# Kernel tuning notes

Hardware: AMD Instinct MI355X
Metric: run time of the kernel (lower is better)

## Reference

```python
import jax, jax.numpy as jnp
import numpy as np

DIM = 2048
N_HEADS = 16
HEAD_DIM = DIM // N_HEADS
B, S = 2, 2048


def apply_rotary(x, cos, sin):
    # x: [..., dim]; cos/sin broadcast to [..., dim//2]
    # even/odd interleaved rotation, matching the torch ::2 / 1::2 indexing
    xe = x[..., 0::2]
    xo = x[..., 1::2]
    oe = xe * cos - xo * sin
    oo = xo * cos + xe * sin
    return jnp.stack([oe, oo], axis=-1).reshape(x.shape)


def setup_inputs() -> dict:
    key = jax.random.key(0)
    ks = jax.random.split(key, 12)
    scale = 1.0 / np.sqrt(DIM)
    x = jax.random.normal(ks[0], (B, S, DIM), dtype=jnp.float32)
    cos = jax.random.normal(ks[1], (S, DIM // 2), dtype=jnp.float32)
    sin = jax.random.normal(ks[2], (S, DIM // 2), dtype=jnp.float32)
    mask = jnp.zeros((1, 1, S, S), dtype=jnp.float32)
    Wq = jax.random.normal(ks[3], (DIM, DIM), dtype=jnp.float32) * scale
    bq = jnp.zeros((DIM,), dtype=jnp.float32)
    Wk = jax.random.normal(ks[4], (DIM, DIM), dtype=jnp.float32) * scale
    bk = jnp.zeros((DIM,), dtype=jnp.float32)
    Wv = jax.random.normal(ks[5], (DIM, DIM), dtype=jnp.float32) * scale
    bv = jnp.zeros((DIM,), dtype=jnp.float32)
    Wo = jax.random.normal(ks[6], (DIM, DIM), dtype=jnp.float32) * scale
    bo = jnp.zeros((DIM,), dtype=jnp.float32)
    return {"x": x, "cos": cos, "sin": sin, "mask": mask,
            "Wq": Wq, "bq": bq, "Wk": Wk, "bk": bk,
            "Wv": Wv, "bv": bv, "Wo": Wo, "bo": bo}


def reference(x, cos, sin, mask, Wq, bq, Wk, bk, Wv, bv, Wo, bo):
    # Linear projections (torch nn.Linear: y = x @ W.T + b)
    q = jnp.einsum('bsd,ed->bse', x, Wq) + bq
    k = jnp.einsum('bsd,ed->bse', x, Wk) + bk
    v = jnp.einsum('bsd,ed->bse', x, Wv) + bv
    # RoPE on full dim, then split into heads (faithful to source ordering)
    q = apply_rotary(q, cos, sin).reshape(B, S, N_HEADS, HEAD_DIM)
    k = apply_rotary(k, cos, sin).reshape(B, S, N_HEADS, HEAD_DIM)
    v = v.reshape(B, S, N_HEADS, HEAD_DIM)
    scale = 1.0 / jnp.sqrt(jnp.float32(HEAD_DIM))
    attn = jnp.einsum('bqhd,bkhd->bhqk', q, k) * scale  # [B,H,S,S]
    attn = attn + mask
    attn = jax.nn.softmax(attn, axis=-1)
    out = jnp.einsum('bhqk,bkhd->bqhd', attn, v).reshape(B, S, DIM)
    return jnp.einsum('bsd,ed->bse', out, Wo) + bo
```

## Files before the change

### kernel.cpp

```cpp
#include <hip/hip_runtime.h>

#define DIM   2048
#define SLEN  2048
#define BATCH 2
#define NHEAD 16
#define HDIM  128
#define MROWS (BATCH*SLEN)

typedef __attribute__((ext_vector_type(8))) __bf16 bf16x8;
typedef __attribute__((ext_vector_type(4))) float  f32x4;
typedef __attribute__((ext_vector_type(8))) unsigned short u16x8;
typedef __attribute__((ext_vector_type(4))) unsigned short u16x4;

__device__ __forceinline__ unsigned short f2bf(float f) {
  union { float f; unsigned u; } v; v.f = f;
  unsigned r = v.u + 0x7FFFu + ((v.u >> 16) & 1u);
  return (unsigned short)(r >> 16);
}
__device__ __forceinline__ float bf2f(unsigned short h) {
  union { unsigned u; float f; } v; v.u = ((unsigned)h) << 16;
  return v.f;
}
__device__ __forceinline__ void gload16(const void* g, void* l) {
  __builtin_amdgcn_global_load_lds(
      (const __attribute__((address_space(1))) void*)g,
      (__attribute__((address_space(3))) void*)l, 16, 0, 0);
}

__global__ __launch_bounds__(256) void conv_f32_bf16(
    const float* __restrict__ in, unsigned short* __restrict__ out, int n4) {
  int t = blockIdx.x * 256 + threadIdx.x;
  if (t >= n4) return;
  f32x4 v = *(const f32x4*)(in + (size_t)t * 4);
  u16x4 o;
  o[0] = f2bf(v[0]); o[1] = f2bf(v[1]); o[2] = f2bf(v[2]); o[3] = f2bf(v[3]);
  *(u16x4*)(out + (size_t)t * 4) = o;
}

template<int OUT_MODE>
__global__ __launch_bounds__(256) void gemm_bt(
    const unsigned short* __restrict__ A,
    const unsigned short* __restrict__ Bw,
    const float* __restrict__ bias,
    void* __restrict__ Cout, int M, int N, int K)
{
  __shared__ __align__(16) unsigned short As[128][32];
  __shared__ __align__(16) unsigned short Bs[128][32];
  const int tid  = threadIdx.x;
  const int lane = tid & 63;
  const int wid  = tid >> 6;
  const int wr   = wid >> 1, wc = wid & 1;
  const int lrow = lane >> 4, lcol = lane & 15;

  const int gx = gridDim.x;
  int bid = blockIdx.y * gx + blockIdx.x;
  int nwg = gx * gridDim.y;
  int swz = (bid & 7) * (nwg >> 3) + (bid >> 3);
  const int row0 = (swz % gx) * 128, col0 = (swz / gx) * 128;

  f32x4 acc[4][4] = {};

  const unsigned short* Ablk = A  + (size_t)row0 * K;
  const unsigned short* Bblk = Bw + (size_t)col0 * K;
  char* AsB = (char*)&As[0][0];
  char* BsB = (char*)&Bs[0][0];

  for (int k0 = 0; k0 < K; k0 += 32) {
#pragma unroll
    for (int r = 0; r < 2; ++r) {
      int f = r * 256 + tid;
      gload16(Ablk + (size_t)(f >> 2) * K + k0 + (f & 3) * 8, AsB + (r * 256 + wid * 64) * 16);
      gload16(Bblk + (size_t)(f >> 2) * K + k0 + (f & 3) * 8, BsB + (r * 256 + wid * 64) * 16);
    }
    __syncthreads();
    bf16x8 af[4], bfv[4];
#pragma unroll
    for (int m = 0; m < 4; ++m)
      af[m] = *(const bf16x8*)&As[wr * 64 + m * 16 + lcol][lrow * 8];
#pragma unroll
    for (int n = 0; n < 4; ++n)
      bfv[n] = *(const bf16x8*)&Bs[wc * 64 + n * 16 + lcol][lrow * 8];
#pragma unroll
    for (int m = 0; m < 4; ++m)
#pragma unroll
      for (int n = 0; n < 4; ++n)
        acc[m][n] = __builtin_amdgcn_mfma_f32_16x16x32_bf16(af[m], bfv[n], acc[m][n], 0, 0, 0);
    __syncthreads();
  }

#pragma unroll
  for (int m = 0; m < 4; ++m) {
#pragma unroll
    for (int n = 0; n < 4; ++n) {
      int col = col0 + wc * 64 + n * 16 + lcol;
      float bv = bias[col];
      if (OUT_MODE == 2) {
        int row = row0 + wr * 64 + m * 16 + lrow * 4;
        u16x4 o;
#pragma unroll
        for (int j = 0; j < 4; ++j) o[j] = f2bf(acc[m][n][j] + bv);
        *(u16x4*)((unsigned short*)Cout +
                  ((size_t)((row >> 11) * DIM + col)) * SLEN + (row & (SLEN - 1))) = o;
      } else {
#pragma unroll
        for (int j = 0; j < 4; ++j) {
          int row = row0 + wr * 64 + m * 16 + lrow * 4 + j;
          float val = acc[m][n][j] + bv;
          if (OUT_MODE == 1) ((unsigned short*)Cout)[(size_t)row * N + col] = f2bf(val);
          else               ((float*)Cout)[(size_t)row * N + col] = val;
        }
      }
    }
  }
}

__global__ __launch_bounds__(256) void gemm_qkv(
    const unsigned short* __restrict__ A,
    const unsigned short* __restrict__ Bw3,
    const float* __restrict__ bq, const float* __restrict__ bk, const float* __restrict__ bv,
    unsigned short* __restrict__ qout,
    unsigned short* __restrict__ kout,
    unsigned short* __restrict__ vtout)
{
  __shared__ __align__(16) unsigned short As[128][32];
  __shared__ __align__(16) unsigned short Bs[128][32];
  const int tid  = threadIdx.x;
  const int lane = tid & 63;
  const int wid  = tid >> 6;
  const int wr   = wid >> 1, wc = wid & 1;
  const int lrow = lane >> 4, lcol = lane & 15;

  int bid = blockIdx.y * 32 + blockIdx.x;
  int swz = (bid & 7) * 192 + (bid >> 3);
  const int row0 = (swz & 31) * 128;
  const int by   = swz >> 5;
  const int seg  = by >> 4;
  const int col0 = (by & 15) * 128;

  f32x4 acc[4][4] = {};

  const unsigned short* Ablk = A   + (size_t)row0 * DIM;
  const unsigned short* Bblk = Bw3 + (size_t)by * 128 * DIM;
  char* AsB = (char*)&As[0][0];
  char* BsB = (char*)&Bs[0][0];

  for (int k0 = 0; k0 < DIM; k0 += 32) {
#pragma unroll
    for (int r = 0; r < 2; ++r) {
      int f = r * 256 + tid;
      gload16(Ablk + (size_t)(f >> 2) * DIM + k0 + (f & 3) * 8, AsB + (r * 256 + wid * 64) * 16);
      gload16(Bblk + (size_t)(f >> 2) * DIM + k0 + (f & 3) * 8, BsB + (r * 256 + wid * 64) * 16);
    }
    __syncthreads();
    bf16x8 af[4], bfv[4];
#pragma unroll
    for (int m = 0; m < 4; ++m)
      af[m] = *(const bf16x8*)&As[wr * 64 + m * 16 + lcol][lrow * 8];
#pragma unroll
    for (int n = 0; n < 4; ++n)
      bfv[n] = *(const bf16x8*)&Bs[wc * 64 + n * 16 + lcol][lrow * 8];
#pragma unroll
    for (int m = 0; m < 4; ++m)
#pragma unroll
      for (int n = 0; n < 4; ++n)
        acc[m][n] = __builtin_amdgcn_mfma_f32_16x16x32_bf16(af[m], bfv[n], acc[m][n], 0, 0, 0);
    __syncthreads();
  }

  const float* bias = (seg == 0) ? bq : (seg == 1) ? bk : bv;
#pragma unroll
  for (int m = 0; m < 4; ++m) {
#pragma unroll
    for (int n = 0; n < 4; ++n) {
      int col = col0 + wc * 64 + n * 16 + lcol;
      float bvv = bias[col];
      if (seg == 2) {
        int row = row0 + wr * 64 + m * 16 + lrow * 4;
        u16x4 o;
#pragma unroll
        for (int j = 0; j < 4; ++j) o[j] = f2bf(acc[m][n][j] + bvv);
        *(u16x4*)(vtout + ((size_t)((row >> 11) * DIM + col)) * SLEN + (row & (SLEN - 1))) = o;
      } else {
        unsigned short* out = (seg == 0) ? qout : kout;
#pragma unroll
        for (int j = 0; j < 4; ++j) {
          int row = row0 + wr * 64 + m * 16 + lrow * 4 + j;
          out[(size_t)row * DIM + col] = f2bf(acc[m][n][j] + bvv);
        }
      }
    }
  }
}

__global__ __launch_bounds__(256) void rope_inplace(
    unsigned short* __restrict__ q,
    const float* __restrict__ cosT, const float* __restrict__ sinT, float scale) {
  int t   = blockIdx.x * 256 + threadIdx.x;
  int row = t >> 8;
  int e0  = (t & 255) * 8;
  int s   = row & (SLEN - 1);
  unsigned short* p = q + (size_t)row * DIM + e0;
  u16x8 v = *(u16x8*)p;
  f32x4 c  = *(const f32x4*)(cosT + (size_t)s * (DIM / 2) + (e0 >> 1));
  f32x4 sn = *(const f32x4*)(sinT + (size_t)s * (DIM / 2) + (e0 >> 1));
#pragma unroll
  for (int i = 0; i < 4; ++i) {
    float xe = bf2f(v[2 * i]), xo = bf2f(v[2 * i + 1]);
    float oe = (xe * c[i] - xo * sn[i]) * scale;
    float oo = (xo * c[i] + xe * sn[i]) * scale;
    v[2 * i] = f2bf(oe); v[2 * i + 1] = f2bf(oo);
  }
  *(u16x8*)p = v;
}

__global__ __launch_bounds__(256) void attn_fwd(
    const unsigned short* __restrict__ Q,
    const unsigned short* __restrict__ Kg,
    const unsigned short* __restrict__ VtG,
    const float* __restrict__ mask,
    unsigned short* __restrict__ O)
{
  __shared__ __align__(16) unsigned short Ks[64][128];
  __shared__ __align__(16) unsigned short Vts[128][64];
  __shared__ __align__(16) unsigned short Ps[4][16][64];

  const int qt = blockIdx.x, h = blockIdx.y, b = blockIdx.z;
  const int tid = threadIdx.x, lane = tid & 63, wid = tid >> 6;
  const int lrow = lane >> 4, lcol = lane & 15;
  const int sx = (lcol & 7) << 4;

  const unsigned short* Qb  = Q  + ((size_t)(b * SLEN + qt * 64)) * DIM + h * HDIM;
  const unsigned short* Kb  = Kg + (size_t)(b * SLEN) * DIM + h * HDIM;
  const unsigned short* Vtb = VtG + ((size_t)(b * DIM + h * HDIM)) * SLEN;
  const float* maskRow = mask + (size_t)(qt * 64 + wid * 16 + lcol) * SLEN;

  bf16x8 qf[4];
#pragma unroll
  for (int kk = 0; kk < 4; ++kk)
    qf[kk] = *(const bf16x8*)(Qb + (size_t)(wid * 16 + lcol) * DIM + kk * 32 + lrow * 8);

  float m_run = -1e30f, l_run = 0.f;
  f32x4 acc_o[8] = {};

  char* KsB  = (char*)&Ks[0][0];
  char* VtsB = (char*)&Vts[0][0];
  char* PsB  = (char*)&Ps[0][0][0];

  for (int kt = 0; kt < SLEN / 64; ++kt) {
    __syncthreads();
#pragma unroll
    for (int r = 0; r < 4; ++r) {
      int L = r * 256 + wid * 64 + lane;
      int krow = L >> 4, kc = (L & 15) ^ (krow & 7);
      gload16(Kb + (size_t)(kt * 64 + krow) * DIM + kc * 8,
              KsB + (size_t)(r * 256 + wid * 64) * 16);
    }
#pragma unroll
    for (int r = 0; r < 4; ++r) {
      int L = r * 256 + wid * 64 + lane;
      int d = L >> 3, vc = (L & 7) ^ (d & 7);
      gload16(Vtb + (size_t)d * SLEN + kt * 64 + vc * 8,
              VtsB + (size_t)(r * 256 + wid * 64) * 16);
    }
    __syncthreads();

    f32x4 sacc[4] = {};
#pragma unroll
    for (int kn = 0; kn < 4; ++kn)
#pragma unroll
      for (int kk = 0; kk < 4; ++kk) {
        bf16x8 kf = *(const bf16x8*)(KsB + (size_t)(kn * 16 + lcol) * 256
                                         + ((kk * 64 + lrow * 16) ^ sx));
        sacc[kn] = __builtin_amdgcn_mfma_f32_16x16x32_bf16(kf, qf[kk], sacc[kn], 0, 0, 0);
      }

    float sv[16];
#pragma unroll
    for (int kn = 0; kn < 4; ++kn) {
      f32x4 mv = *(const f32x4*)(maskRow + kt * 64 + kn * 16 + lrow * 4);
#pragma unroll
      for (int r = 0; r < 4; ++r) sv[kn * 4 + r] = sacc[kn][r] + mv[r];
    }

    float pmax = sv[0];
#pragma unroll
    for (int i = 1; i < 16; ++i) pmax = fmaxf(pmax, sv[i]);
    pmax = fmaxf(pmax, __shfl_xor(pmax, 16, 64));
    pmax = fmaxf(pmax, __shfl_xor(pmax, 32, 64));

    if (!__all(pmax - m_run <= 8.0f)) {
      float mnew = fmaxf(m_run, pmax);
      float alpha = __expf(m_run - mnew);
      m_run = mnew;
      l_run *= alpha;
      float ar[4];
#pragma unroll
      for (int r = 0; r < 4; ++r) ar[r] = __shfl(alpha, lrow * 4 + r, 64);
#pragma unroll
      for (int d = 0; d < 8; ++d) {
        f32x4 t = acc_o[d];
#pragma unroll
        for (int r = 0; r < 4; ++r) t[r] *= ar[r];
        acc_o[d] = t;
      }
    }

    float pv[16];
    float rsum = 0.f;
#pragma unroll
    for (int i = 0; i < 16; ++i) { float pe = __expf(sv[i] - m_run); pv[i] = pe; rsum += pe; }
    rsum += __shfl_xor(rsum, 16, 64);
    rsum += __shfl_xor(rsum, 32, 64);
    l_run += rsum;

#pragma unroll
    for (int kn = 0; kn < 4; ++kn)
#pragma unroll
      for (int r = 0; r < 4; ++r)
        *(unsigned short*)(PsB + wid * 2048 + lcol * 128
                           + ((kn * 32 + (lrow * 4 + r) * 2) ^ sx)) = f2bf(pv[kn * 4 + r]);

    bf16x8 pf[2];
#pragma unroll
    for (int ks = 0; ks < 2; ++ks)
      pf[ks] = *(const bf16x8*)(PsB + wid * 2048 + lcol * 128
                                + ((ks * 64 + lrow * 16) ^ sx));
#pragma unroll
    for (int d = 0; d < 8; ++d)
#pragma unroll
      for (int ks = 0; ks < 2; ++ks) {
        bf16x8 vf = *(const bf16x8*)(VtsB + (size_t)(d * 16 + lcol) * 128
                                          + ((ks * 64 + lrow * 16) ^ sx));
        acc_o[d] = __builtin_amdgcn_mfma_f32_16x16x32_bf16(pf[ks], vf, acc_o[d], 0, 0, 0);
      }
  }

  float linv[4];
#pragma unroll
  for (int r = 0; r < 4; ++r) linv[r] = 1.0f / __shfl(l_run, lrow * 4 + r, 64);
  int orow0 = b * SLEN + qt * 64 + wid * 16 + lrow * 4;
#pragma unroll
  for (int d = 0; d < 8; ++d)
#pragma unroll
    for (int r = 0; r < 4; ++r) {
      float o = acc_o[d][r] * linv[r];
      O[(size_t)(orow0 + r) * DIM + h * HDIM + d * 16 + lcol] = f2bf(o);
    }
}

extern "C" void kernel_launch(void* const* d_in, const int* in_sizes, int n_in,
                              void* d_out, int out_size, void* d_ws, size_t ws_size,
                              hipStream_t stream) {
  const float* x    = (const float*)d_in[0];
  const float* cosT = (const float*)d_in[1];
  const float* sinT = (const float*)d_in[2];
  const float* mask = (const float*)d_in[3];
  const float* Wq   = (const float*)d_in[4];
  const float* bq   = (const float*)d_in[5];
  const float* Wk   = (const float*)d_in[6];
  const float* bk   = (const float*)d_in[7];
  const float* Wv   = (const float*)d_in[8];
  const float* bv   = (const float*)d_in[9];
  const float* Wo   = (const float*)d_in[10];
  const float* bo   = (const float*)d_in[11];

  const size_t MB = 1u << 20;
  if (ws_size < 72 * MB) return;

  char* ws = (char*)d_ws;
  unsigned short* xb = (unsigned short*)(ws);
  unsigned short* qb = (unsigned short*)(ws + 16 * MB);
  unsigned short* kb = (unsigned short*)(ws + 32 * MB);
  unsigned short* Vt = (unsigned short*)(ws + 48 * MB);
  unsigned short* Ob = xb;

  const float scale = 0.08838834764831845f;
  conv_f32_bf16<<<8192, 256, 0, stream>>>(x, xb, (MROWS * DIM) / 4);

  if (ws_size >= 88 * MB) {
    unsigned short* Wb3 = (unsigned short*)(ws + 64 * MB);
    conv_f32_bf16<<<4096, 256, 0, stream>>>(Wq, Wb3, (DIM * DIM) / 4);
    conv_f32_bf16<<<4096, 256, 0, stream>>>(Wk, Wb3 + (size_t)DIM * DIM, (DIM * DIM) / 4);
    conv_f32_bf16<<<4096, 256, 0, stream>>>(Wv, Wb3 + (size_t)2 * DIM * DIM, (DIM * DIM) / 4);
    gemm_qkv<<<dim3(MROWS / 128, 48), 256, 0, stream>>>(xb, Wb3, bq, bk, bv, qb, kb, Vt);
    rope_inplace<<<4096, 256, 0, stream>>>(qb, cosT, sinT, scale);
    rope_inplace<<<4096, 256, 0, stream>>>(kb, cosT, sinT, 1.0f);
    attn_fwd<<<dim3(SLEN / 64, NHEAD, BATCH), 256, 0, stream>>>(qb, kb, Vt, mask, Ob);
    conv_f32_bf16<<<4096, 256, 0, stream>>>(Wo, Wb3, (DIM * DIM) / 4);
    gemm_bt<0><<<dim3(MROWS / 128, DIM / 128), 256, 0, stream>>>(Ob, Wb3, bo, d_out, MROWS, DIM, DIM);
  } else {
    unsigned short* Wb = (unsigned short*)(ws + 64 * MB);
    dim3 gGemm(MROWS / 128, DIM / 128);
    conv_f32_bf16<<<4096, 256, 0, stream>>>(Wq, Wb, (DIM * DIM) / 4);
    gemm_bt<1><<<gGemm, 256, 0, stream>>>(xb, Wb, bq, qb, MROWS, DIM, DIM);
    conv_f32_bf16<<<4096, 256, 0, stream>>>(Wk, Wb, (DIM * DIM) / 4);
    gemm_bt<1><<<gGemm, 256, 0, stream>>>(xb, Wb, bk, kb, MROWS, DIM, DIM);
    conv_f32_bf16<<<4096, 256, 0, stream>>>(Wv, Wb, (DIM * DIM) / 4);
    gemm_bt<2><<<gGemm, 256, 0, stream>>>(xb, Wb, bv, Vt, MROWS, DIM, DIM);
    rope_inplace<<<4096, 256, 0, stream>>>(qb, cosT, sinT, scale);
    rope_inplace<<<4096, 256, 0, stream>>>(kb, cosT, sinT, 1.0f);
    attn_fwd<<<dim3(SLEN / 64, NHEAD, BATCH), 256, 0, stream>>>(qb, kb, Vt, mask, Ob);
    conv_f32_bf16<<<4096, 256, 0, stream>>>(Wo, Wb, (DIM * DIM) / 4);
    gemm_bt<0><<<gGemm, 256, 0, stream>>>(Ob, Wb, bo, d_out, MROWS, DIM, DIM);
  }
}
```

Before: 415.5 us.

## Fuse RoPE into QKV GEMM epilogue and swizzle attention block order

The rotary embedding and Q scaling move into the QKV GEMM epilogue. Each lane swaps even/odd column values with a lane xor-shuffle, reads cos/sin and rotates before the bf16 store. This removes two separate in-place RoPE kernels and their read-modify-write passes over Q and K. The attention grid is also remapped so that consecutive blocks spread across heads and batches, which changes cache locality and XCD assignment. Cost: the epilogue now does scalar cos/sin gathers per element, and the fused rotation rounds to bf16 once instead of twice, which changes numerics slightly.

```diff
diff --git a/kernel.cpp b/kernel.cpp
--- a/kernel.cpp
+++ b/kernel.cpp
@@ -118,6 +118,7 @@
     const unsigned short* __restrict__ A,
     const unsigned short* __restrict__ Bw3,
     const float* __restrict__ bq, const float* __restrict__ bk, const float* __restrict__ bv,
+    const float* __restrict__ cosT, const float* __restrict__ sinT, float qscale,
     unsigned short* __restrict__ qout,
     unsigned short* __restrict__ kout,
     unsigned short* __restrict__ vtout)
@@ -167,25 +168,42 @@
     __syncthreads();
   }
 
-  const float* bias = (seg == 0) ? bq : (seg == 1) ? bk : bv;
-#pragma unroll
-  for (int m = 0; m < 4; ++m) {
-#pragma unroll
-    for (int n = 0; n < 4; ++n) {
-      int col = col0 + wc * 64 + n * 16 + lcol;
-      float bvv = bias[col];
-      if (seg == 2) {
+  if (seg == 2) {
+#pragma unroll
+    for (int m = 0; m < 4; ++m) {
+#pragma unroll
+      for (int n = 0; n < 4; ++n) {
+        int col = col0 + wc * 64 + n * 16 + lcol;
+        float bvv = bv[col];
         int row = row0 + wr * 64 + m * 16 + lrow * 4;
         u16x4 o;
 #pragma unroll
         for (int j = 0; j < 4; ++j) o[j] = f2bf(acc[m][n][j] + bvv);
         *(u16x4*)(vtout + ((size_t)((row >> 11) * DIM + col)) * SLEN + (row & (SLEN - 1))) = o;
-      } else {
-        unsigned short* out = (seg == 0) ? qout : kout;
+      }
+    }
+  } else {
+    unsigned short* out = (seg == 0) ? qout : kout;
+    const float* bias   = (seg == 0) ? bq : bk;
+    const float  osc    = (seg == 0) ? qscale : 1.0f;
+#pragma unroll
+    for (int m = 0; m < 4; ++m) {
+#pragma unroll
+      for (int n = 0; n < 4; ++n) {
+        int col = col0 + wc * 64 + n * 16 + lcol;
+        float bvv = bias[col];
+        int ip  = col >> 1;
+        int odd = col & 1;
 #pragma unroll
         for (int j = 0; j < 4; ++j) {
           int row = row0 + wr * 64 + m * 16 + lrow * 4 + j;
-          out[(size_t)row * DIM + col] = f2bf(acc[m][n][j] + bvv);
+          int s   = row & (SLEN - 1);
+          float v = acc[m][n][j] + bvv;
+          float p = __shfl_xor(v, 1, 64);
+          float c  = cosT[(size_t)s * (DIM / 2) + ip];
+          float sn = sinT[(size_t)s * (DIM / 2) + ip];
+          float o  = odd ? (v * c + p * sn) : (v * c - p * sn);
+          out[(size_t)row * DIM + col] = f2bf(o * osc);
         }
       }
     }
@@ -224,7 +242,12 @@
   __shared__ __align__(16) unsigned short Vts[128][64];
   __shared__ __align__(16) unsigned short Ps[4][16][64];
 
-  const int qt = blockIdx.x, h = blockIdx.y, b = blockIdx.z;
+  int s0 = blockIdx.x + 32 * (blockIdx.y + 16 * blockIdx.z);
+  int xc = s0 & 7, jj = s0 >> 3;
+  int pane = xc * 4 + (jj >> 5);
+  const int qt = jj & 31;
+  const int h  = pane & 15, b = pane >> 4;
+
   const int tid = threadIdx.x, lane = tid & 63, wid = tid >> 6;
   const int lrow = lane >> 4, lcol = lane & 15;
   const int sx = (lcol & 7) << 4;
@@ -382,9 +405,8 @@
     conv_f32_bf16<<<4096, 256, 0, stream>>>(Wq, Wb3, (DIM * DIM) / 4);
     conv_f32_bf16<<<4096, 256, 0, stream>>>(Wk, Wb3 + (size_t)DIM * DIM, (DIM * DIM) / 4);
     conv_f32_bf16<<<4096, 256, 0, stream>>>(Wv, Wb3 + (size_t)2 * DIM * DIM, (DIM * DIM) / 4);
-    gemm_qkv<<<dim3(MROWS / 128, 48), 256, 0, stream>>>(xb, Wb3, bq, bk, bv, qb, kb, Vt);
-    rope_inplace<<<4096, 256, 0, stream>>>(qb, cosT, sinT, scale);
-    rope_inplace<<<4096, 256, 0, stream>>>(kb, cosT, sinT, 1.0f);
+    gemm_qkv<<<dim3(MROWS / 128, 48), 256, 0, stream>>>(xb, Wb3, bq, bk, bv,
+                                                        cosT, sinT, scale, qb, kb, Vt);
     attn_fwd<<<dim3(SLEN / 64, NHEAD, BATCH), 256, 0, stream>>>(qb, kb, Vt, mask, Ob);
     conv_f32_bf16<<<4096, 256, 0, stream>>>(Wo, Wb3, (DIM * DIM) / 4);
     gemm_bt<0><<<dim3(MROWS / 128, DIM / 128), 256, 0, stream>>>(Ob, Wb3, bo, d_out, MROWS, DIM, DIM);
```

Measured after the change: 404.2 us. -2.7%, faster.
